# Kernel tuning notes

Measured on AMD Instinct MI355X. Metric: run time of the kernel, lower is better.

Reference implementation:

```python
import jax, jax.numpy as jnp
import numpy as np
import math

N_FFT = 1024
HOP = 256
N_FREQ = N_FFT // 2 + 1  # 513
B = 16
T_FRAMES = 4000


def _hann_periodic(n_fft):
    n = np.arange(n_fft, dtype=np.float32)
    return (0.5 - 0.5 * np.cos(2.0 * np.pi * n / n_fft)).astype(np.float32)


def setup_inputs() -> dict:
    key = jax.random.key(0)
    k1, k2, k3 = jax.random.split(key, 3)
    mag = jax.random.uniform(k1, (B, N_FREQ, T_FRAMES), dtype=jnp.float32)
    cos_phase = jax.random.normal(k2, (B, N_FREQ, T_FRAMES), dtype=jnp.float32)
    sin_phase = jax.random.normal(k3, (B, N_FREQ, T_FRAMES), dtype=jnp.float32)
    window = jnp.asarray(_hann_periodic(N_FFT))
    return {"mag": mag, "cos_phase": cos_phase, "sin_phase": sin_phase, "window": window}


def _make_basis(n_fft):
    # Real DFT synthesis basis with Hermitian-symmetry scaling, matching the torch module.
    n_freq = n_fft // 2 + 1
    n = jnp.arange(n_fft, dtype=jnp.float32)
    k = jnp.arange(n_freq, dtype=jnp.float32)
    angles = 2.0 * math.pi * n[:, None] * k[None, :] / n_fft  # [n_fft, n_freq]
    scale = jnp.full((n_freq,), 2.0 / n_fft, dtype=jnp.float32)
    scale = scale.at[0].set(1.0 / n_fft)
    if n_fft % 2 == 0:
        scale = scale.at[-1].set(1.0 / n_fft)
    cos_b = jnp.cos(angles) * scale[None, :]  # [n_fft, n_freq]
    sin_b = jnp.sin(angles) * scale[None, :]
    return cos_b, sin_b


def reference(mag, cos_phase, sin_phase, window):
    n_fft = window.shape[0]
    cos_b, sin_b = _make_basis(n_fft)
    S_real = mag * cos_phase  # [B, F, T]
    S_imag = mag * sin_phase
    # frames[b,t,n] = sum_f S_real[b,f,t]*cos_b[n,f] - S_imag[b,f,t]*sin_b[n,f]
    frames = jnp.einsum('bft,nf->btn', S_real, cos_b) - jnp.einsum('bft,nf->btn', S_imag, sin_b)
    frames = frames * window[None, None, :]  # [B, T, n_fft]
    Bn, T, N = frames.shape
    out_len = (T - 1) * HOP + n_fft
    # Overlap-add via a single scatter-add (duplicate indices accumulate).
    flat_idx = (jnp.arange(T)[:, None] * HOP + jnp.arange(n_fft)[None, :]).reshape(-1)  # [T*N]
    audio = jnp.zeros((Bn, out_len), dtype=frames.dtype).at[:, flat_idx].add(frames.reshape(Bn, -1))
    win_sq = window * window
    win_env = jnp.zeros((out_len,), dtype=frames.dtype).at[flat_idx].add(jnp.tile(win_sq, T))
    audio = audio / (win_env[None, :] + 1e-11)
    c = n_fft // 2
    return audio[:, c:-c]  # [B, (T-1)*HOP]
```

## Files before the change

### kernel.cpp

```cpp
#include <hip/hip_runtime.h>
#include <hip/hip_bf16.h>


#define NFFT   1024
#define NFREQ  513
#define TFR    4000
#define NB     16
#define HOP    256
#define OUTLEN 1023744
#define KPAD   1088
#define IMB    544
#define PADR   4160
#define K2     4352

typedef __bf16 bf16x8 __attribute__((ext_vector_type(8)));
typedef float  f32x4  __attribute__((ext_vector_type(4)));
typedef unsigned short ushort8 __attribute__((ext_vector_type(8)));

__device__ inline unsigned short f2bf(float x) {
    unsigned u = __float_as_uint(x);
    unsigned r = (u + 0x7FFFu + ((u >> 16) & 1u)) >> 16;
    return (unsigned short)r;
}

__global__ __launch_bounds__(256) void prep_s(
        const float* __restrict__ mag, const float* __restrict__ cosp,
        const float* __restrict__ sinp, unsigned short* __restrict__ S) {
    const int f0 = blockIdx.x * 32, t0 = blockIdx.y * 64, b = blockIdx.z;
    __shared__ float Lr[32][65];
    __shared__ float Li[32][65];
    const int tid = threadIdx.x;
    const int tt = tid & 63, kq = tid >> 6;
    const size_t bst = (size_t)NFREQ * TFR;
    const float* magB = mag  + (size_t)b * bst;
    const float* cosB = cosp + (size_t)b * bst;
    const float* sinB = sinp + (size_t)b * bst;
    const int t = t0 + tt - 1;
    #pragma unroll
    for (int u = 0; u < 8; ++u) {
        const int kk = kq * 8 + u;
        const int f = f0 + kk;
        float vr = 0.f, vi = 0.f;
        if (f < NFREQ && t >= 0 && t < TFR) {
            const size_t i = (size_t)f * TFR + t;
            const float m = magB[i];
            vr = m * cosB[i];
            vi = m * sinB[i];
        }
        Lr[kk][tt] = vr;
        Li[kk][tt] = vi;
    }
    __syncthreads();
    const int tt2 = tid >> 2, kk0 = (tid & 3) * 8;
    ushort8 pr, pi;
    #pragma unroll
    for (int j = 0; j < 8; ++j) {
        pr[j] = f2bf(Lr[kk0 + j][tt2]);
        pi[j] = f2bf(Li[kk0 + j][tt2]);
    }
    unsigned short* rowp = S + ((size_t)b * PADR + t0 + tt2) * KPAD;
    *(ushort8*)(rowp + f0 + kk0)       = pr;
    *(ushort8*)(rowp + IMB + f0 + kk0) = pi;
}

__global__ void build_basis2(const float* __restrict__ window,
                             unsigned short* __restrict__ bas2) {
    const int j = blockIdx.x;
    const float step = 6.28318530717958647692f / (float)NFFT;
    #pragma unroll
    for (int sec = 0; sec < 4; ++sec) {
        const int n = j + 256 * sec;
        const float wv = window[n];
        for (int f = threadIdx.x; f < KPAD; f += 256) {
            float v = 0.f;
            if (f < NFREQ) {
                const float scale = (f == 0 || f == NFFT / 2) ? (1.f / NFFT) : (2.f / NFFT);
                v = cosf(step * (float)((n * f) & (NFFT - 1))) * scale * wv;
            } else if (f >= IMB && f < IMB + NFREQ) {
                const int ff = f - IMB;
                const float scale = (ff == 0 || ff == NFFT / 2) ? (1.f / NFFT) : (2.f / NFFT);
                v = -sinf(step * (float)((n * ff) & (NFFT - 1))) * scale * wv;
            }
            bas2[(size_t)j * K2 + sec * KPAD + f] = f2bf(v);
        }
    }
}

__global__ __launch_bounds__(256) void gemm_ola(
        const unsigned short* __restrict__ S, const unsigned short* __restrict__ bas2,
        const float* __restrict__ window, float* __restrict__ out) {
    const int lin  = (blockIdx.z * 32 + blockIdx.y) * 2 + blockIdx.x;
    const int logi = (lin & 7) * 128 + (lin >> 3);
    const int b    = logi >> 6;
    const int tile = (logi & 63) >> 1;
    const int j0   = (logi & 1) * 128;
    const int th0  = 2 + tile * 128;

    __shared__ unsigned short As[128 * 32];
    __shared__ unsigned short Bs[128 * 32];
    const int tid = threadIdx.x;
    const int lane = tid & 63, wave = tid >> 6;
    const int wr = wave >> 1, wc = wave & 1;
    const int quad = lane >> 4, r16 = lane & 15;

    const unsigned short* Sb = S + (size_t)b * PADR * KPAD;

    f32x4 acc[4][4];
    #pragma unroll
    for (int mi = 0; mi < 4; ++mi)
        #pragma unroll
        for (int ni = 0; ni < 4; ++ni)
            acc[mi][ni] = 0.f;

    const int ldrow = lane >> 2;
    const int ko    = (lane & 3) * 8;

    for (int sec = 0; sec < 4; ++sec) {
        const unsigned short* Ssec = Sb + (size_t)(th0 + 1 - sec) * KPAD;
        const unsigned short* Bsec = bas2 + (size_t)j0 * K2 + sec * KPAD;
        for (int fs = 0; fs < KPAD / 32; ++fs) {
            const int kc = fs * 32 + ko;
            #pragma unroll
            for (int i = 0; i < 2; ++i) {
                const int chunk = wave * 2 + i;
                const int row = chunk * 16 + ldrow;
                __builtin_amdgcn_global_load_lds(
                    (const __attribute__((address_space(1))) void*)(Ssec + (size_t)row * KPAD + kc),
                    (__attribute__((address_space(3))) void*)(As + chunk * 512 + lane * 8),
                    16, 0, 0);
                __builtin_amdgcn_global_load_lds(
                    (const __attribute__((address_space(1))) void*)(Bsec + (size_t)row * K2 + kc),
                    (__attribute__((address_space(3))) void*)(Bs + chunk * 512 + lane * 8),
                    16, 0, 0);
            }
            __syncthreads();
            bf16x8 af[4], bfr[4];
            #pragma unroll
            for (int mi = 0; mi < 4; ++mi)
                af[mi] = *(const bf16x8*)(As + (wr * 64 + mi * 16 + r16) * 32 + quad * 8);
            #pragma unroll
            for (int ni = 0; ni < 4; ++ni)
                bfr[ni] = *(const bf16x8*)(Bs + (wc * 64 + ni * 16 + r16) * 32 + quad * 8);
            #pragma unroll
            for (int mi = 0; mi < 4; ++mi)
                #pragma unroll
                for (int ni = 0; ni < 4; ++ni)
                    acc[mi][ni] = __builtin_amdgcn_mfma_f32_16x16x32_bf16(
                        af[mi], bfr[ni], acc[mi][ni], 0, 0, 0);
            __syncthreads();
        }
    }

    float* outB = out + (size_t)b * OUTLEN;
    float wsq[4][4];
    #pragma unroll
    for (int ni = 0; ni < 4; ++ni) {
        const int j = j0 + wc * 64 + ni * 16 + r16;
        #pragma unroll
        for (int k = 0; k < 4; ++k) {
            const float w = window[j + 256 * k];
            wsq[ni][k] = w * w;
        }
    }
    const int thb = th0 + wr * 64 + quad * 4;
    if (th0 >= 3 && th0 + 127 <= TFR - 1) {
        float inv[4];
        #pragma unroll
        for (int ni = 0; ni < 4; ++ni)
            inv[ni] = 1.f / (wsq[ni][0] + wsq[ni][1] + wsq[ni][2] + wsq[ni][3] + 1e-11f);
        #pragma unroll
        for (int ni = 0; ni < 4; ++ni) {
            const int j = j0 + wc * 64 + ni * 16 + r16;
            #pragma unroll
            for (int mi = 0; mi < 4; ++mi) {
                #pragma unroll
                for (int reg = 0; reg < 4; ++reg) {
                    const int th = thb + mi * 16 + reg;
                    outB[th * HOP + j - 512] = acc[mi][ni][reg] * inv[ni];
                }
            }
        }
    } else {
        #pragma unroll
        for (int ni = 0; ni < 4; ++ni) {
            const int j = j0 + wc * 64 + ni * 16 + r16;
            #pragma unroll
            for (int mi = 0; mi < 4; ++mi) {
                #pragma unroll
                for (int reg = 0; reg < 4; ++reg) {
                    const int th = thb + mi * 16 + reg;
                    if (th <= TFR) {
                        float env = 1e-11f;
                        #pragma unroll
                        for (int k = 0; k < 4; ++k)
                            if ((unsigned)(th - k) < (unsigned)TFR) env += wsq[ni][k];
                        outB[th * HOP + j - 512] = acc[mi][ni][reg] / env;
                    }
                }
            }
        }
    }
}

extern "C" void kernel_launch(void* const* d_in, const int* in_sizes, int n_in,
                              void* d_out, int out_size, void* d_ws, size_t ws_size,
                              hipStream_t stream) {
    const float* mag    = (const float*)d_in[0];
    const float* cosp   = (const float*)d_in[1];
    const float* sinp   = (const float*)d_in[2];
    const float* window = (const float*)d_in[3];
    float* out = (float*)d_out;

    unsigned short* S    = (unsigned short*)d_ws;
    unsigned short* bas2 = S + (size_t)NB * PADR * KPAD;

    prep_s<<<dim3(17, PADR / 64, NB), 256, 0, stream>>>(mag, cosp, sinp, S);
    build_basis2<<<256, 256, 0, stream>>>(window, bas2);
    gemm_ola<<<dim3(2, 32, NB), 256, 0, stream>>>(S, bas2, window, out);
}
```

Baseline: 611.4 us.

## Share one A tile across all four overlap sections per K step

The four section loops are merged into a single K loop. Each step loads a 136-row A tile once, plus the B tiles for all four sections into a larger XOR-swizzled LDS buffer, then runs the four sections' MFMAs using row-shifted views of the shared A tile. This cuts redundant global loads of the overlapping S rows and quarters the number of barriers. In exchange, LDS use rises to about 41 KB per block, which may lower occupancy, and more bytes are loaded per barrier.

```diff
diff --git a/kernel.cpp b/kernel.cpp
--- a/kernel.cpp
+++ b/kernel.cpp
@@ -96,14 +96,16 @@
     const int j0   = (logi & 1) * 128;
     const int th0  = 2 + tile * 128;
 
-    __shared__ unsigned short As[128 * 32];
-    __shared__ unsigned short Bs[128 * 32];
+    __shared__ unsigned short As[136 * 32];
+    __shared__ unsigned short Bs[128 * 128];
     const int tid = threadIdx.x;
     const int lane = tid & 63, wave = tid >> 6;
     const int wr = wave >> 1, wc = wave & 1;
     const int quad = lane >> 4, r16 = lane & 15;
 
-    const unsigned short* Sb = S + (size_t)b * PADR * KPAD;
+    const unsigned short* Sb  = S + (size_t)b * PADR * KPAD;
+    const unsigned short* Ap0 = Sb + (size_t)(th0 - 2) * KPAD;
+    const unsigned short* Bp0 = bas2 + (size_t)j0 * K2;
 
     f32x4 acc[4][4];
     #pragma unroll
@@ -112,43 +114,55 @@
         for (int ni = 0; ni < 4; ++ni)
             acc[mi][ni] = 0.f;
 
-    const int ldrow = lane >> 2;
-    const int ko    = (lane & 3) * 8;
-
-    for (int sec = 0; sec < 4; ++sec) {
-        const unsigned short* Ssec = Sb + (size_t)(th0 + 1 - sec) * KPAD;
-        const unsigned short* Bsec = bas2 + (size_t)j0 * K2 + sec * KPAD;
-        for (int fs = 0; fs < KPAD / 32; ++fs) {
-            const int kc = fs * 32 + ko;
-            #pragma unroll
-            for (int i = 0; i < 2; ++i) {
-                const int chunk = wave * 2 + i;
-                const int row = chunk * 16 + ldrow;
-                __builtin_amdgcn_global_load_lds(
-                    (const __attribute__((address_space(1))) void*)(Ssec + (size_t)row * KPAD + kc),
-                    (__attribute__((address_space(3))) void*)(As + chunk * 512 + lane * 8),
-                    16, 0, 0);
-                __builtin_amdgcn_global_load_lds(
-                    (const __attribute__((address_space(1))) void*)(Bsec + (size_t)row * K2 + kc),
-                    (__attribute__((address_space(3))) void*)(Bs + chunk * 512 + lane * 8),
-                    16, 0, 0);
-            }
-            __syncthreads();
+    for (int fs = 0; fs < KPAD / 32; ++fs) {
+        const int kb = fs * 32;
+        #pragma unroll
+        for (int h = 0; h < 2; ++h) {
+            const int slot = h * 256 + tid;
+            const int row = slot >> 2, c16 = slot & 3;
+            __builtin_amdgcn_global_load_lds(
+                (const __attribute__((address_space(1))) void*)(Ap0 + (size_t)row * KPAD + kb + c16 * 8),
+                (__attribute__((address_space(3))) void*)(As + slot * 8),
+                16, 0, 0);
+        }
+        if (tid < 32) {
+            const int slot = 512 + tid;
+            const int row = slot >> 2, c16 = slot & 3;
+            __builtin_amdgcn_global_load_lds(
+                (const __attribute__((address_space(1))) void*)(Ap0 + (size_t)row * KPAD + kb + c16 * 8),
+                (__attribute__((address_space(3))) void*)(As + slot * 8),
+                16, 0, 0);
+        }
+        #pragma unroll
+        for (int h = 0; h < 8; ++h) {
+            const int slot = h * 256 + tid;
+            const int row  = slot >> 4;
+            const int m16  = (slot & 15) ^ (row & 7);
+            const int sec  = m16 >> 2, c16 = m16 & 3;
+            __builtin_amdgcn_global_load_lds(
+                (const __attribute__((address_space(1))) void*)(Bp0 + (size_t)row * K2 + sec * KPAD + kb + c16 * 8),
+                (__attribute__((address_space(3))) void*)(Bs + slot * 8),
+                16, 0, 0);
+        }
+        __syncthreads();
+        #pragma unroll
+        for (int s = 0; s < 4; ++s) {
             bf16x8 af[4], bfr[4];
             #pragma unroll
             for (int mi = 0; mi < 4; ++mi)
-                af[mi] = *(const bf16x8*)(As + (wr * 64 + mi * 16 + r16) * 32 + quad * 8);
+                af[mi] = *(const bf16x8*)(As + (wr * 64 + mi * 16 + r16 + 3 - s) * 32 + quad * 8);
             #pragma unroll
             for (int ni = 0; ni < 4; ++ni)
-                bfr[ni] = *(const bf16x8*)(Bs + (wc * 64 + ni * 16 + r16) * 32 + quad * 8);
+                bfr[ni] = *(const bf16x8*)(Bs + (wc * 64 + ni * 16 + r16) * 128
+                                              + (((s * 4 + quad) ^ (r16 & 7)) * 8));
             #pragma unroll
             for (int mi = 0; mi < 4; ++mi)
                 #pragma unroll
                 for (int ni = 0; ni < 4; ++ni)
                     acc[mi][ni] = __builtin_amdgcn_mfma_f32_16x16x32_bf16(
                         af[mi], bfr[ni], acc[mi][ni], 0, 0, 0);
-            __syncthreads();
-        }
+        }
+        __syncthreads();
     }
 
     float* outB = out + (size_t)b * OUTLEN;
```

New measurement: 546.8 us. 10.6% less time.
